# Optimization experiments

Hardware: AMD Instinct MI355X
Metric: run time of the kernel (lower is better)

Reference implementation:

```python
import jax, jax.numpy as jnp
import numpy as np
import math

N_HEADS = 16
DIM = 1024
D_HEAD = DIM // N_HEADS
BS, QLEN = 2, 2048


def setup_inputs() -> dict:
    key = jax.random.key(0)
    ks = jax.random.split(key, 10)
    s = 0.02
    return {
        "input": jax.random.normal(ks[0], (BS, QLEN, DIM), dtype=jnp.float32),
        "mask": jnp.ones((BS, QLEN), dtype=jnp.int32),
        "q_w": jax.random.normal(ks[1], (DIM, DIM), dtype=jnp.float32) * s,
        "q_b": jax.random.normal(ks[2], (DIM,), dtype=jnp.float32) * s,
        "k_w": jax.random.normal(ks[3], (DIM, DIM), dtype=jnp.float32) * s,
        "k_b": jax.random.normal(ks[4], (DIM,), dtype=jnp.float32) * s,
        "v_w": jax.random.normal(ks[5], (DIM, DIM), dtype=jnp.float32) * s,
        "v_b": jax.random.normal(ks[6], (DIM,), dtype=jnp.float32) * s,
        "o_w": jax.random.normal(ks[7], (DIM, DIM), dtype=jnp.float32) * s,
        "o_b": jax.random.normal(ks[8], (DIM,), dtype=jnp.float32) * s,
    }


def _shape(x, bs):
    # (bs, len, dim) -> (bs, heads, len, d_head)
    return x.reshape(bs, -1, N_HEADS, D_HEAD).transpose(0, 2, 1, 3)


def reference(input, mask, q_w, q_b, k_w, k_b, v_w, v_b, o_w, o_b):
    bs, qlen, dim = input.shape
    # projections (torch Linear: x @ W^T + b)
    q = _shape(input @ q_w.T + q_b, bs)
    k = _shape(input @ k_w.T + k_b, bs)
    v = _shape(input @ v_w.T + v_b, bs)
    q = q / math.sqrt(D_HEAD)
    # scores: (bs, heads, qlen, klen)
    scores = jnp.einsum("bhqd,bhkd->bhqk", q, k)
    pad = (mask == 0)[:, None, None, :]  # (bs,1,1,klen)
    scores = jnp.where(pad, -jnp.inf, scores)
    weights = jax.nn.softmax(scores.astype(jnp.float32), axis=-1).astype(scores.dtype)
    # dropout p=0.0 (eval) -> identity
    context = jnp.einsum("bhqk,bhkd->bhqd", weights, v)
    context = context.transpose(0, 2, 1, 3).reshape(bs, qlen, dim)
    return context @ o_w.T + o_b
```

## Files before the change

### kernel.cpp

```cpp
#include <hip/hip_runtime.h>


#define BS    2
#define QLEN  2048
#define DIM   1024
#define NH    16
#define DH    64
#define MTOK  (BS * QLEN)

#define QSCALE 0.18033688011112042f

typedef __attribute__((ext_vector_type(8))) short short8;
typedef __attribute__((ext_vector_type(4))) float float4_t;
typedef __attribute__((ext_vector_type(4))) int   int4_t;

__device__ __forceinline__ ushort f2bf(float f) {
    unsigned u = __float_as_uint(f);
    return (ushort)((u + 0x7fffu + ((u >> 16) & 1u)) >> 16);
}
__device__ __forceinline__ short8 pack8(float4 a0, float4 a1) {
    short8 r;
    r[0] = (short)f2bf(a0.x); r[1] = (short)f2bf(a0.y);
    r[2] = (short)f2bf(a0.z); r[3] = (short)f2bf(a0.w);
    r[4] = (short)f2bf(a1.x); r[5] = (short)f2bf(a1.y);
    r[6] = (short)f2bf(a1.z); r[7] = (short)f2bf(a1.w);
    return r;
}

__device__ __forceinline__ void glds16(const void* g, void* l) {
    __builtin_amdgcn_global_load_lds(
        (const __attribute__((address_space(1))) unsigned int*)g,
        (__attribute__((address_space(3))) unsigned int*)l, 16, 0, 0);
}

__global__ __launch_bounds__(256) void conv_all(
    const float* __restrict__ x,  const float* __restrict__ qw,
    const float* __restrict__ kw, const float* __restrict__ vw,
    const float* __restrict__ ow,
    ushort* __restrict__ Xbf, ushort* __restrict__ Wbf)
{
    const int blk = blockIdx.x;
    const float* s; ushort* d; size_t base;
    if (blk < 4096)      { s = x;  d = Xbf;             base = (size_t)blk * 1024; }
    else if (blk < 5120) { s = qw; d = Wbf;             base = (size_t)(blk - 4096) * 1024; }
    else if (blk < 6144) { s = kw; d = Wbf + 1048576;   base = (size_t)(blk - 5120) * 1024; }
    else if (blk < 7168) { s = vw; d = Wbf + 2097152;   base = (size_t)(blk - 6144) * 1024; }
    else                 { s = ow; d = Wbf + 3145728;   base = (size_t)(blk - 7168) * 1024; }
    const size_t i = base + threadIdx.x * 4;
    float4 v = *(const float4*)(s + i);
    ushort4 o;
    o.x = f2bf(v.x); o.y = f2bf(v.y); o.z = f2bf(v.z); o.w = f2bf(v.w);
    *(ushort4*)(d + i) = o;
}

__global__ __launch_bounds__(256) void transpose_v(
    const ushort* __restrict__ Vrow, ushort* __restrict__ Vt)
{
    __shared__ ushort T[64][72];
    const int tid  = threadIdx.x;
    const int tile = blockIdx.x;
    const int bh   = blockIdx.y;
    const int b = bh >> 4, h = bh & 15;

    #pragma unroll
    for (int rep = 0; rep < 2; ++rep) {
        int ch = tid + rep * 256;
        int tok = ch >> 3, seg = ch & 7;
        uint4 v = *(const uint4*)(Vrow + (size_t)(b * QLEN + tile * 64 + tok) * DIM
                                        + h * DH + seg * 8);
        *(uint4*)&T[tok][seg * 8] = v;
    }
    __syncthreads();
    #pragma unroll
    for (int rep = 0; rep < 2; ++rep) {
        int ch = tid + rep * 256;
        int dim = ch >> 3, tseg = ch & 7;
        ushort t0 = T[tseg * 8 + 0][dim], t1 = T[tseg * 8 + 1][dim];
        ushort t2 = T[tseg * 8 + 2][dim], t3 = T[tseg * 8 + 3][dim];
        ushort t4 = T[tseg * 8 + 4][dim], t5 = T[tseg * 8 + 5][dim];
        ushort t6 = T[tseg * 8 + 6][dim], t7 = T[tseg * 8 + 7][dim];
        uint4 o;
        o.x = (unsigned)t0 | ((unsigned)t1 << 16);
        o.y = (unsigned)t2 | ((unsigned)t3 << 16);
        o.z = (unsigned)t4 | ((unsigned)t5 << 16);
        o.w = (unsigned)t6 | ((unsigned)t7 << 16);
        *(uint4*)(Vt + (size_t)bh * DH * QLEN + (size_t)dim * QLEN
                      + tile * 64 + tseg * 8) = o;
    }
}

__global__ __launch_bounds__(256) void gemm_qkv(
    const ushort* __restrict__ A, const ushort* __restrict__ Bw,
    const float* __restrict__ bias0, const float* __restrict__ bias1,
    const float* __restrict__ bias2,
    ushort* __restrict__ outQ, ushort* __restrict__ outK, ushort* __restrict__ outVt)
{
    __shared__ ushort As[2][128 * 32];
    __shared__ ushort Bs[2][128 * 32];
    const int tid  = threadIdx.x;
    const int w    = tid >> 6;
    const int lane = tid & 63;
    const int r15  = lane & 15;
    const int quad = lane >> 4;
    const int xcd = blockIdx.x & 7;
    const int lid = blockIdx.x >> 3;
    const int brow = (xcd & 3) * 8  + (lid & 7);
    const int bcol = (xcd >> 2) * 12 + (lid >> 3);
    const int wrow = (w >> 1) * 64;
    const int wcol = (w & 1) * 64;
    const int K = DIM;

    float4_t acc[4][4];
    #pragma unroll
    for (int i = 0; i < 4; ++i)
        #pragma unroll
        for (int j = 0; j < 4; ++j)
            acc[i][j] = (float4_t){0.f, 0.f, 0.f, 0.f};

    int chS[2];
    const ushort* gaS[2];
    const ushort* gbS[2];
    #pragma unroll
    for (int rep = 0; rep < 2; ++rep) {
        const int ch  = w * 128 + rep * 64 + lane;
        const int row = ch >> 2;
        const int g   = (ch & 3) ^ ((row >> 1) & 3);
        chS[rep] = ch;
        gaS[rep] = A  + (size_t)(brow * 128 + row) * K + g * 8;
        gbS[rep] = Bw + (size_t)(bcol * 128 + row) * K + g * 8;
    }
    const int ph = (quad ^ ((r15 >> 1) & 3)) * 8;

    #pragma unroll
    for (int rep = 0; rep < 2; ++rep) {
        glds16(gaS[rep], &As[0][chS[rep] * 8]);
        glds16(gbS[rep], &Bs[0][chS[rep] * 8]);
    }
    __syncthreads();

    int p = 0;
    for (int k0 = 0; k0 < K; k0 += 32) {
        if (k0 + 32 < K) {
            #pragma unroll
            for (int rep = 0; rep < 2; ++rep) {
                glds16(gaS[rep] + k0 + 32, &As[p ^ 1][chS[rep] * 8]);
                glds16(gbS[rep] + k0 + 32, &Bs[p ^ 1][chS[rep] * 8]);
            }
        }
        short8 af[4], bf[4];
        #pragma unroll
        for (int ms = 0; ms < 4; ++ms)
            af[ms] = *(const short8*)&As[p][(wrow + ms * 16 + r15) * 32 + ph];
        #pragma unroll
        for (int ns = 0; ns < 4; ++ns)
            bf[ns] = *(const short8*)&Bs[p][(wcol + ns * 16 + r15) * 32 + ph];
        #pragma unroll
        for (int ms = 0; ms < 4; ++ms)
            #pragma unroll
            for (int ns = 0; ns < 4; ++ns)
                acc[ms][ns] = __builtin_amdgcn_mfma_f32_16x16x32_bf16(
                    af[ms], bf[ns], acc[ms][ns], 0, 0, 0);
        __syncthreads();
        p ^= 1;
    }

    #pragma unroll
    for (int ms = 0; ms < 4; ++ms) {
        const int rowg = brow * 128 + wrow + ms * 16 + quad * 4;
        #pragma unroll
        for (int ns = 0; ns < 4; ++ns) {
            const int colg = bcol * 128 + wcol + ns * 16 + r15;
            if (colg < 1024) {
                const float bb = bias0[colg];
                #pragma unroll
                for (int r = 0; r < 4; ++r)
                    outQ[(size_t)(rowg + r) * 1024 + colg] =
                        f2bf((acc[ms][ns][r] + bb) * QSCALE);
            } else if (colg < 2048) {
                const float bb = bias1[colg - 1024];
                #pragma unroll
                for (int r = 0; r < 4; ++r)
                    outK[(size_t)(rowg + r) * 1024 + (colg - 1024)] =
                        f2bf(acc[ms][ns][r] + bb);
            } else {
                const int vcol = colg - 2048;
                const int hh = vcol >> 6, dd = vcol & 63;
                const float bb = bias2[vcol];
                const int bidx = rowg >> 11;
                const int tloc = rowg & 2047;
                ushort4 o4;
                o4.x = f2bf(acc[ms][ns][0] + bb);
                o4.y = f2bf(acc[ms][ns][1] + bb);
                o4.z = f2bf(acc[ms][ns][2] + bb);
                o4.w = f2bf(acc[ms][ns][3] + bb);
                *(ushort4*)&outVt[((size_t)(bidx * 16 + hh) * 64 + dd) * QLEN + tloc] = o4;
            }
        }
    }
}

__global__ __launch_bounds__(256) void gemm_o(
    const ushort* __restrict__ A, const ushort* __restrict__ Bw,
    const float* __restrict__ bias, float* __restrict__ Out)
{
    __shared__ ushort As[2][128 * 64];
    __shared__ ushort Bs[2][64 * 64];
    const int tid  = threadIdx.x;
    const int w    = tid >> 6;
    const int lane = tid & 63;
    const int r15  = lane & 15;
    const int quad = lane >> 4;
    const int xcd = blockIdx.x & 7;
    const int lid = blockIdx.x >> 3;
    const int brow = (xcd & 3) * 8 + (lid & 7);
    const int bcol = (xcd >> 2) * 8 + (lid >> 3);
    const int wrow = w * 32;
    const int K = DIM;

    float4_t acc[2][4];
    #pragma unroll
    for (int i = 0; i < 2; ++i)
        #pragma unroll
        for (int j = 0; j < 4; ++j)
            acc[i][j] = (float4_t){0.f, 0.f, 0.f, 0.f};

    int chA[4];  const ushort* gaS[4];
    #pragma unroll
    for (int rep = 0; rep < 4; ++rep) {
        const int ch  = w * 256 + rep * 64 + lane;
        const int row = ch >> 3;
        const int g   = (ch & 7) ^ (row & 7);
        chA[rep] = ch;
        gaS[rep] = A + (size_t)(brow * 128 + row) * K + g * 8;
    }
    int chB[2];  const ushort* gbS[2];
    #pragma unroll
    for (int rep = 0; rep < 2; ++rep) {
        const int ch  = w * 128 + rep * 64 + lane;
        const int row = ch >> 3;
        const int g   = (ch & 7) ^ (row & 7);
        chB[rep] = ch;
        gbS[rep] = Bw + (size_t)(bcol * 64 + row) * K + g * 8;
    }
    const int xg = r15 & 7;

    #pragma unroll
    for (int rep = 0; rep < 4; ++rep)
        glds16(gaS[rep], &As[0][chA[rep] * 8]);
    #pragma unroll
    for (int rep = 0; rep < 2; ++rep)
        glds16(gbS[rep], &Bs[0][chB[rep] * 8]);
    __syncthreads();

    int p = 0;
    for (int k0 = 0; k0 < K; k0 += 64) {
        if (k0 + 64 < K) {
            #pragma unroll
            for (int rep = 0; rep < 4; ++rep)
                glds16(gaS[rep] + k0 + 64, &As[p ^ 1][chA[rep] * 8]);
            #pragma unroll
            for (int rep = 0; rep < 2; ++rep)
                glds16(gbS[rep] + k0 + 64, &Bs[p ^ 1][chB[rep] * 8]);
        }
        #pragma unroll
        for (int hh = 0; hh < 2; ++hh) {
            const int ph = ((hh * 4 + quad) ^ xg) * 8;
            short8 af[2], bf[4];
            #pragma unroll
            for (int ms = 0; ms < 2; ++ms)
                af[ms] = *(const short8*)&As[p][(wrow + ms * 16 + r15) * 64 + ph];
            #pragma unroll
            for (int ns = 0; ns < 4; ++ns)
                bf[ns] = *(const short8*)&Bs[p][(ns * 16 + r15) * 64 + ph];
            #pragma unroll
            for (int ms = 0; ms < 2; ++ms)
                #pragma unroll
                for (int ns = 0; ns < 4; ++ns)
                    acc[ms][ns] = __builtin_amdgcn_mfma_f32_16x16x32_bf16(
                        af[ms], bf[ns], acc[ms][ns], 0, 0, 0);
        }
        __syncthreads();
        p ^= 1;
    }

    #pragma unroll
    for (int ms = 0; ms < 2; ++ms) {
        const int rowg = brow * 128 + wrow + ms * 16 + quad * 4;
        #pragma unroll
        for (int ns = 0; ns < 4; ++ns) {
            const int colg = bcol * 64 + ns * 16 + r15;
            const float bb = bias[colg];
            #pragma unroll
            for (int r = 0; r < 4; ++r)
                Out[(size_t)(rowg + r) * 1024 + colg] = acc[ms][ns][r] + bb;
        }
    }
}

__global__ __launch_bounds__(256) void gemm_f32in_bf16out(
    const float* __restrict__ X, const float* __restrict__ W,
    const float* __restrict__ B, ushort* __restrict__ Out,
    int M, int N, int K, float scale)
{
    const int lane = threadIdx.x & 63;
    const int wid  = (blockIdx.x * blockDim.x + threadIdx.x) >> 6;
    const int tilesN = N >> 4;
    const int tm = wid / tilesN;
    const int tn = wid - tm * tilesN;
    const int r15  = lane & 15;
    const int quad = lane >> 4;

    const float* xp = X + (size_t)(tm * 16 + r15) * K + quad * 8;
    const float* wp = W + (size_t)(tn * 16 + r15) * K + quad * 8;

    float4_t acc = {0.f, 0.f, 0.f, 0.f};
    for (int k0 = 0; k0 < K; k0 += 32) {
        float4 a0 = *(const float4*)(xp + k0);
        float4 a1 = *(const float4*)(xp + k0 + 4);
        float4 b0 = *(const float4*)(wp + k0);
        float4 b1 = *(const float4*)(wp + k0 + 4);
        acc = __builtin_amdgcn_mfma_f32_16x16x32_bf16(pack8(a0, a1), pack8(b0, b1), acc, 0, 0, 0);
    }
    const int col  = tn * 16 + r15;
    const float bias = B[col];
    const int row0 = tm * 16 + quad * 4;
    #pragma unroll
    for (int r = 0; r < 4; ++r)
        Out[(size_t)(row0 + r) * N + col] = f2bf((acc[r] + bias) * scale);
}

__global__ __launch_bounds__(256) void gemm_bf16in_f32out(
    const ushort* __restrict__ X, const float* __restrict__ W,
    const float* __restrict__ B, float* __restrict__ Out,
    int M, int N, int K)
{
    const int lane = threadIdx.x & 63;
    const int wid  = (blockIdx.x * blockDim.x + threadIdx.x) >> 6;
    const int tilesN = N >> 4;
    const int tm = wid / tilesN;
    const int tn = wid - tm * tilesN;
    const int r15  = lane & 15;
    const int quad = lane >> 4;

    const ushort* xp = X + (size_t)(tm * 16 + r15) * K + quad * 8;
    const float*  wp = W + (size_t)(tn * 16 + r15) * K + quad * 8;

    float4_t acc = {0.f, 0.f, 0.f, 0.f};
    for (int k0 = 0; k0 < K; k0 += 32) {
        short8 a = *(const short8*)(xp + k0);
        float4 b0 = *(const float4*)(wp + k0);
        float4 b1 = *(const float4*)(wp + k0 + 4);
        acc = __builtin_amdgcn_mfma_f32_16x16x32_bf16(a, pack8(b0, b1), acc, 0, 0, 0);
    }
    const int col  = tn * 16 + r15;
    const float bias = B[col];
    const int row0 = tm * 16 + quad * 4;
    #pragma unroll
    for (int r = 0; r < 4; ++r)
        Out[(size_t)(row0 + r) * N + col] = acc[r] + bias;
}

__global__ __launch_bounds__(256, 2) void flash_attn(
    const ushort* __restrict__ Qb, const ushort* __restrict__ Kb,
    const ushort* __restrict__ Vt, const int* __restrict__ mask,
    ushort* __restrict__ Cb)
{
    __shared__ __align__(16) ushort Ks[2][64][64];
    __shared__ __align__(16) ushort Vs[4][64][64];
    __shared__ __align__(16) float  Mb[QLEN];

    const int tid  = threadIdx.x;
    const int w    = tid >> 6;
    const int lane = tid & 63;
    const int r15  = lane & 15;
    const int quad = lane >> 4;
    const int flat = blockIdx.x;
    const int xcd  = flat & 7;
    const int j    = flat >> 3;
    const int bh   = xcd + 8 * (j >> 4);
    const int qt   = j & 15;
    const int b = bh >> 4, h = bh & 15;

    {
        const int4* m4 = (const int4*)(mask + b * QLEN);
        #pragma unroll
        for (int rep = 0; rep < 2; ++rep) {
            const int idx = tid + rep * 256;
            int4 mv = m4[idx];
            float4 o;
            o.x = mv.x ? 0.f : -INFINITY;
            o.y = mv.y ? 0.f : -INFINITY;
            o.z = mv.z ? 0.f : -INFINITY;
            o.w = mv.w ? 0.f : -INFINITY;
            *(float4*)&Mb[idx * 4] = o;
        }
    }

    const int qbase = qt * 128 + w * 32;
    const ushort* qp = Qb + (size_t)(b * QLEN + qbase + r15) * DIM + h * DH + quad * 8;
    short8 qf[2][2];
    qf[0][0] = *(const short8*)(qp);
    qf[0][1] = *(const short8*)(qp + 32);
    qf[1][0] = *(const short8*)(qp + 16 * DIM);
    qf[1][1] = *(const short8*)(qp + 16 * DIM + 32);

    const ushort* kg = Kb + (size_t)b * QLEN * DIM + h * DH;
    const ushort* vg = Vt + (size_t)bh * DH * QLEN;

    const int a0 = tid >> 3, seg = tid & 7;
    const int krow0 = (((a0 & 7) >> 2) << 4) + (((a0 >> 3) & 3) << 2) + (a0 & 3);
    const int sK = (seg ^ (krow0 & 7)) << 3;
    const int sV = (seg ^ (a0 & 7)) << 3;
    const int xq = (quad ^ (r15 & 7)) << 3;

    float4_t o[2][4];
    float4_t ol[2];
    #pragma unroll
    for (int rg = 0; rg < 2; ++rg) {
        ol[rg] = (float4_t){0.f, 0.f, 0.f, 0.f};
        #pragma unroll
        for (int ds = 0; ds < 4; ++ds)
            o[rg][ds] = (float4_t){0.f, 0.f, 0.f, 0.f};
    }
    short8 ones8;
    #pragma unroll
    for (int i = 0; i < 8; ++i) ones8[i] = (short)0x3F80;

    uint4 kr0, kr1, vr0, vr1;
    int pkA[4][2][2], pkB[4][2][2];

#define LOAD_TILE(KT) do {                                                    \
    kr0 = *(const uint4*)(kg + (size_t)((KT) + a0     ) * DIM  + seg * 8);    \
    kr1 = *(const uint4*)(kg + (size_t)((KT) + a0 + 32) * DIM  + seg * 8);    \
    vr0 = *(const uint4*)(vg + (size_t)(a0     ) * QLEN + (KT) + seg * 8);    \
    vr1 = *(const uint4*)(vg + (size_t)(a0 + 32) * QLEN + (KT) + seg * 8);    \
} while (0)

#define STORE_TILE(KBUF, VBUF) do {                                           \
    *(uint4*)&Ks[KBUF][krow0     ][sK] = kr0;                                 \
    *(uint4*)&Ks[KBUF][krow0 + 32][sK] = kr1;                                 \
    *(uint4*)&Vs[VBUF][a0        ][sV] = vr0;                                 \
    *(uint4*)&Vs[VBUF][a0 + 32   ][sV] = vr1;                                 \
} while (0)

#define S_PHASE(KBUF, KT, PK) do {                                            \
    _Pragma("unroll")                                                         \
    for (int ks = 0; ks < 4; ++ks) {                                          \
        const ushort* krow = &Ks[KBUF][ks * 16 + r15][0];                     \
        short8 kf0 = *(const short8*)(krow + xq);                             \
        short8 kf1 = *(const short8*)(krow + (xq ^ 32));                      \
        const float4 mb = *(const float4*)&Mb[(KT) + ((ks >> 1) << 5)         \
                                              + (quad << 3) + ((ks & 1) << 2)]; \
        _Pragma("unroll")                                                     \
        for (int rg = 0; rg < 2; ++rg) {                                      \
            float4_t s = {0.f, 0.f, 0.f, 0.f};                                \
            s = __builtin_amdgcn_mfma_f32_16x16x32_bf16(kf0, qf[rg][0], s, 0, 0, 0); \
            s = __builtin_amdgcn_mfma_f32_16x16x32_bf16(kf1, qf[rg][1], s, 0, 0, 0); \
            unsigned u0 = __float_as_uint(__builtin_amdgcn_exp2f(s[0] + mb.x)); \
            unsigned u1 = __float_as_uint(__builtin_amdgcn_exp2f(s[1] + mb.y)); \
            unsigned u2 = __float_as_uint(__builtin_amdgcn_exp2f(s[2] + mb.z)); \
            unsigned u3 = __float_as_uint(__builtin_amdgcn_exp2f(s[3] + mb.w)); \
            PK[ks][rg][0] = __builtin_amdgcn_perm(u1, u0, 0x07060302);        \
            PK[ks][rg][1] = __builtin_amdgcn_perm(u3, u2, 0x07060302);        \
        }                                                                     \
    }                                                                         \
} while (0)

#define PV_PHASE(VBUF, PK) do {                                               \
    _Pragma("unroll")                                                         \
    for (int ck = 0; ck < 2; ++ck) {                                          \
        short8 vf[4];                                                         \
        _Pragma("unroll")                                                     \
        for (int ds = 0; ds < 4; ++ds)                                        \
            vf[ds] = *(const short8*)(&Vs[VBUF][ds * 16 + r15][0] + (xq ^ (ck << 5))); \
        _Pragma("unroll")                                                     \
        for (int rg = 0; rg < 2; ++rg) {                                      \
            int4_t pfi = { PK[2 * ck][rg][0], PK[2 * ck][rg][1],              \
                           PK[2 * ck + 1][rg][0], PK[2 * ck + 1][rg][1] };    \
            short8 pf = __builtin_bit_cast(short8, pfi);                      \
            _Pragma("unroll")                                                 \
            for (int ds = 0; ds < 4; ++ds)                                    \
                o[rg][ds] = __builtin_amdgcn_mfma_f32_16x16x32_bf16(          \
                    pf, vf[ds], o[rg][ds], 0, 0, 0);                          \
            ol[rg] = __builtin_amdgcn_mfma_f32_16x16x32_bf16(                 \
                pf, ones8, ol[rg], 0, 0, 0);                                  \
        }                                                                     \
    }                                                                         \
} while (0)

    LOAD_TILE(0);
    STORE_TILE(0, 0);
    LOAD_TILE(64);
    __syncthreads();
    S_PHASE(0, 0, pkA);
    STORE_TILE(1, 1);
    __syncthreads();
    LOAD_TILE(128);

    for (int kb = 0; kb < 1792; kb += 256) {
        S_PHASE(1, kb + 64, pkB);  PV_PHASE(0, pkA);
        STORE_TILE(0, 2); __syncthreads(); LOAD_TILE(kb + 192);
        S_PHASE(0, kb + 128, pkA); PV_PHASE(1, pkB);
        STORE_TILE(1, 3); __syncthreads(); LOAD_TILE(kb + 256);
        S_PHASE(1, kb + 192, pkB); PV_PHASE(2, pkA);
        STORE_TILE(0, 0); __syncthreads(); LOAD_TILE(kb + 320);
        S_PHASE(0, kb + 256, pkA); PV_PHASE(3, pkB);
        STORE_TILE(1, 1); __syncthreads(); LOAD_TILE(kb + 384);
    }

    S_PHASE(1, 1856, pkB); PV_PHASE(0, pkA);
    STORE_TILE(0, 2); __syncthreads(); LOAD_TILE(1984);
    S_PHASE(0, 1920, pkA); PV_PHASE(1, pkB);
    STORE_TILE(1, 3); __syncthreads();
    S_PHASE(1, 1984, pkB); PV_PHASE(2, pkA);
    PV_PHASE(3, pkB);

#undef LOAD_TILE
#undef STORE_TILE
#undef S_PHASE
#undef PV_PHASE

    #pragma unroll
    for (int rg = 0; rg < 2; ++rg) {
        #pragma unroll
        for (int r = 0; r < 4; ++r) {
            const float ir = 1.f / fmaxf(ol[rg][r], 1e-30f);
            const size_t rb = (size_t)(b * QLEN + qbase + rg * 16 + quad * 4 + r) * DIM
                              + h * DH;
            Cb[rb +  0 + r15] = f2bf(o[rg][0][r] * ir);
            Cb[rb + 16 + r15] = f2bf(o[rg][1][r] * ir);
            Cb[rb + 32 + r15] = f2bf(o[rg][2][r] * ir);
            Cb[rb + 48 + r15] = f2bf(o[rg][3][r] * ir);
        }
    }
}

extern "C" void kernel_launch(void* const* d_in, const int* in_sizes, int n_in,
                              void* d_out, int out_size, void* d_ws, size_t ws_size,
                              hipStream_t stream)
{
    const float* x    = (const float*)d_in[0];
    const int*   mask = (const int*)d_in[1];
    const float* q_w  = (const float*)d_in[2];
    const float* q_b  = (const float*)d_in[3];
    const float* k_w  = (const float*)d_in[4];
    const float* k_b  = (const float*)d_in[5];
    const float* v_w  = (const float*)d_in[6];
    const float* v_b  = (const float*)d_in[7];
    const float* o_w  = (const float*)d_in[8];
    const float* o_b  = (const float*)d_in[9];
    float* out = (float*)d_out;

    const size_t SEG = (size_t)MTOK * DIM;
    ushort* Qbf = (ushort*)d_out;
    ushort* Xbf = Qbf + SEG;
    ushort* Kb  = (ushort*)d_ws;
    ushort* Cb  = Kb + SEG;
    ushort* Vt  = Cb + SEG;
    ushort* Wbf = Vt + SEG;

    const bool big = ws_size >= (size_t)32 * 1024 * 1024;

    if (big) {
        conv_all<<<8192, 256, 0, stream>>>(x, q_w, k_w, v_w, o_w, Xbf, Wbf);
        gemm_qkv<<<(MTOK / 128) * (3072 / 128), 256, 0, stream>>>(
            Xbf, Wbf, q_b, k_b, v_b, Qbf, Kb, Vt);
        flash_attn<<<(QLEN / 128) * (BS * NH), 256, 0, stream>>>(Qbf, Kb, Vt, mask, Cb);
        gemm_o<<<(MTOK / 128) * (DIM / 64), 256, 0, stream>>>(
            Cb, Wbf + 3 * (size_t)(DIM * DIM), o_b, out);
    } else {
        const int tiles   = (MTOK / 16) * (DIM / 16);
        const int gblocks = tiles / 4;
        gemm_f32in_bf16out<<<gblocks, 256, 0, stream>>>(x, q_w, q_b, Qbf, MTOK, DIM, DIM, QSCALE);
        gemm_f32in_bf16out<<<gblocks, 256, 0, stream>>>(x, k_w, k_b, Kb,  MTOK, DIM, DIM, 1.0f);
        gemm_f32in_bf16out<<<gblocks, 256, 0, stream>>>(x, v_w, v_b, Cb,  MTOK, DIM, DIM, 1.0f);
        transpose_v<<<dim3(QLEN / 64, BS * NH), 256, 0, stream>>>(Cb, Vt);
        flash_attn<<<(QLEN / 128) * (BS * NH), 256, 0, stream>>>(Qbf, Kb, Vt, mask, Cb);
        gemm_bf16in_f32out<<<tiles / 4, 256, 0, stream>>>(Cb, o_w, o_b, out, MTOK, DIM, DIM);
    }
}
```

Before: 191.8 us.

## Triple-buffer QKV GEMM LDS stages with explicit vmcnt waits

Converts the QKV projection GEMM main loop from double-buffered to triple-buffered LDS staging. Two tiles are prefetched ahead, and explicit s_waitcnt vmcnt counts with raw barriers replace __syncthreads, so global-to-LDS loads overlap more compute. This costs 50% more shared memory per block, which may reduce occupancy, and it relies on hand-counted vmcnt values being correct.

```diff
diff --git a/kernel.cpp b/kernel.cpp
--- a/kernel.cpp
+++ b/kernel.cpp
@@ -32,6 +32,10 @@
         (const __attribute__((address_space(1))) unsigned int*)g,
         (__attribute__((address_space(3))) unsigned int*)l, 16, 0, 0);
 }
+
+#define QBAR() do { asm volatile("" ::: "memory");                            \
+                    __builtin_amdgcn_s_barrier();                             \
+                    asm volatile("" ::: "memory"); } while (0)
 
 __global__ __launch_bounds__(256) void conv_all(
     const float* __restrict__ x,  const float* __restrict__ qw,
@@ -95,8 +99,8 @@
     const float* __restrict__ bias2,
     ushort* __restrict__ outQ, ushort* __restrict__ outK, ushort* __restrict__ outVt)
 {
-    __shared__ ushort As[2][128 * 32];
-    __shared__ ushort Bs[2][128 * 32];
+    __shared__ ushort As[3][128 * 32];
+    __shared__ ushort Bs[3][128 * 32];
     const int tid  = threadIdx.x;
     const int w    = tid >> 6;
     const int lane = tid & 63;
@@ -131,38 +135,61 @@
     }
     const int ph = (quad ^ ((r15 >> 1) & 3)) * 8;
 
-    #pragma unroll
-    for (int rep = 0; rep < 2; ++rep) {
-        glds16(gaS[rep], &As[0][chS[rep] * 8]);
-        glds16(gbS[rep], &Bs[0][chS[rep] * 8]);
-    }
-    __syncthreads();
-
-    int p = 0;
-    for (int k0 = 0; k0 < K; k0 += 32) {
-        if (k0 + 32 < K) {
-            #pragma unroll
-            for (int rep = 0; rep < 2; ++rep) {
-                glds16(gaS[rep] + k0 + 32, &As[p ^ 1][chS[rep] * 8]);
-                glds16(gbS[rep] + k0 + 32, &Bs[p ^ 1][chS[rep] * 8]);
-            }
-        }
-        short8 af[4], bf[4];
-        #pragma unroll
-        for (int ms = 0; ms < 4; ++ms)
-            af[ms] = *(const short8*)&As[p][(wrow + ms * 16 + r15) * 32 + ph];
-        #pragma unroll
-        for (int ns = 0; ns < 4; ++ns)
-            bf[ns] = *(const short8*)&Bs[p][(wcol + ns * 16 + r15) * 32 + ph];
-        #pragma unroll
-        for (int ms = 0; ms < 4; ++ms)
-            #pragma unroll
-            for (int ns = 0; ns < 4; ++ns)
-                acc[ms][ns] = __builtin_amdgcn_mfma_f32_16x16x32_bf16(
-                    af[ms], bf[ns], acc[ms][ns], 0, 0, 0);
-        __syncthreads();
-        p ^= 1;
-    }
+#define QKV_STAGE(PS, KOFF) do {                                              \
+    _Pragma("unroll")                                                         \
+    for (int rep = 0; rep < 2; ++rep) {                                       \
+        glds16(gaS[rep] + (KOFF), &As[PS][chS[rep] * 8]);                     \
+        glds16(gbS[rep] + (KOFF), &Bs[PS][chS[rep] * 8]);                     \
+    }                                                                         \
+} while (0)
+
+#define QKV_COMP(PC) do {                                                     \
+    short8 af[4], bf[4];                                                      \
+    _Pragma("unroll")                                                         \
+    for (int ms = 0; ms < 4; ++ms)                                            \
+        af[ms] = *(const short8*)&As[PC][(wrow + ms * 16 + r15) * 32 + ph];   \
+    _Pragma("unroll")                                                         \
+    for (int ns = 0; ns < 4; ++ns)                                            \
+        bf[ns] = *(const short8*)&Bs[PC][(wcol + ns * 16 + r15) * 32 + ph];   \
+    _Pragma("unroll")                                                         \
+    for (int ms = 0; ms < 4; ++ms)                                            \
+        _Pragma("unroll")                                                     \
+        for (int ns = 0; ns < 4; ++ns)                                        \
+            acc[ms][ns] = __builtin_amdgcn_mfma_f32_16x16x32_bf16(            \
+                af[ms], bf[ns], acc[ms][ns], 0, 0, 0);                        \
+} while (0)
+
+#define QKV_STEP(PC, PS, KOFF2) do {                                          \
+    QKV_STAGE(PS, KOFF2);                                                     \
+    asm volatile("s_waitcnt vmcnt(8)" ::: "memory");                          \
+    __builtin_amdgcn_s_barrier();                                             \
+    asm volatile("" ::: "memory");                                            \
+    QKV_COMP(PC);                                                             \
+    QBAR();                                                                   \
+} while (0)
+
+    QKV_STAGE(0, 0);
+    QKV_STAGE(1, 32);
+
+    for (int t0 = 0; t0 < 30; t0 += 3) {
+        const int kb = t0 * 32;
+        QKV_STEP(0, 2, kb + 64);
+        QKV_STEP(1, 0, kb + 96);
+        QKV_STEP(2, 1, kb + 128);
+    }
+    asm volatile("s_waitcnt vmcnt(4)" ::: "memory");
+    __builtin_amdgcn_s_barrier();
+    asm volatile("" ::: "memory");
+    QKV_COMP(0);
+    QBAR();
+    asm volatile("s_waitcnt vmcnt(0)" ::: "memory");
+    __builtin_amdgcn_s_barrier();
+    asm volatile("" ::: "memory");
+    QKV_COMP(1);
+
+#undef QKV_STEP
+#undef QKV_COMP
+#undef QKV_STAGE
 
     #pragma unroll
     for (int ms = 0; ms < 4; ++ms) {
```

Result: slower. 196.3 us (+2.4%).
